# Kernel optimization log

Hardware: AMD Instinct MI355X
Metric: run time of the kernel (lower is better)

Reference implementation:

```python
import jax, jax.numpy as jnp
import numpy as np

N_CELL, N_WELL = 200000, 512
E_CC, E_CW = 1600000, 65536
CF, WF, ED, H = 12, 8, 1, 64
NEG_SLOPE = 0.2


def _p(k, shape, fan_in):
    return jax.random.normal(k, shape, jnp.float32) * (1.0 / np.sqrt(fan_in))


def setup_inputs() -> dict:
    key = jax.random.key(0)
    ks = jax.random.split(key, 32)
    d = {}
    d['cell_x'] = jax.random.normal(ks[0], (N_CELL, CF), jnp.float32)
    d['well_x'] = jax.random.normal(ks[1], (N_WELL, WF), jnp.float32)
    d['c2c_edge_attr'] = jax.random.normal(ks[2], (E_CC, ED), jnp.float32)
    d['c2c_edge_index'] = jax.random.randint(ks[3], (2, E_CC), 0, N_CELL)
    cw_src = jax.random.randint(ks[4], (E_CW,), 0, N_CELL)
    cw_dst = jax.random.randint(ks[5], (E_CW,), 0, N_WELL)
    d['c2w_edge_index'] = jnp.stack([cw_src, cw_dst])
    d['W_cell_emb'] = _p(ks[6], (CF, H), CF)
    d['b_cell_emb'] = jnp.zeros((H,), jnp.float32)
    d['W_well_emb'] = _p(ks[7], (WF, H), WF)
    d['b_well_emb'] = jnp.zeros((H,), jnp.float32)
    d['W_edge_emb'] = _p(ks[8], (ED, H), ED)
    d['b_edge_emb'] = jnp.zeros((H,), jnp.float32)
    d['conv_lin'] = _p(ks[9], (3, H, H), H)
    d['conv_lin_edge'] = _p(ks[10], (3, H, H), H)
    d['conv_att_src'] = _p(ks[11], (3, H), H)
    d['conv_att_dst'] = _p(ks[12], (3, H), H)
    d['conv_att_edge'] = _p(ks[13], (3, H), H)
    d['conv_bias'] = jnp.zeros((3, H), jnp.float32)
    d['wc_lin'] = _p(ks[14], (H, H), H)
    d['wc_att_src'] = _p(ks[15], (H,), H)
    d['wc_att_dst'] = _p(ks[16], (H,), H)
    d['wc_bias'] = jnp.zeros((H,), jnp.float32)
    d['mlp_W1'] = _p(ks[17], (H, H), H)
    d['mlp_b1'] = jnp.zeros((H,), jnp.float32)
    d['mlp_W2'] = _p(ks[18], (H, 75), H)
    d['mlp_b2'] = jnp.zeros((75,), jnp.float32)
    return d


def segment_softmax(logits, seg, num_segments):
    m = jax.ops.segment_max(logits, seg, num_segments=num_segments)
    m = jnp.where(jnp.isfinite(m), m, 0.0)  # empty segments -> 0
    e = jnp.exp(logits - m[seg])
    s = jax.ops.segment_sum(e, seg, num_segments=num_segments)
    return e / s[seg]


def gat_layer(h_src, h_dst, src, dst, lin, att_s, att_d, bias, num_dst,
              edge_feat=None, lin_edge=None, att_e=None):
    # PyG GATConv, heads=1, concat=False, add_self_loops=False
    hs = h_src @ lin                      # [Ns, H]
    hd = hs if h_dst is h_src else h_dst @ lin
    alpha = (hs @ att_s)[src] + (hd @ att_d)[dst]  # [E]
    if edge_feat is not None:
        alpha = alpha + (edge_feat @ lin_edge) @ att_e
    alpha = jax.nn.leaky_relu(alpha, NEG_SLOPE)
    p = segment_softmax(alpha, dst, num_dst)       # scatter-softmax per dst
    out = jax.ops.segment_sum(hs[src] * p[:, None], dst, num_segments=num_dst)
    return out + bias


def reference(cell_x, well_x, c2c_edge_attr,
              W_cell_emb, b_cell_emb, W_well_emb, b_well_emb,
              W_edge_emb, b_edge_emb,
              conv_lin, conv_lin_edge, conv_att_src, conv_att_dst,
              conv_att_edge, conv_bias,
              wc_lin, wc_att_src, wc_att_dst, wc_bias,
              mlp_W1, mlp_b1, mlp_W2, mlp_b2,
              c2c_edge_index, c2w_edge_index):
    h_c = cell_x @ W_cell_emb + b_cell_emb
    h_w = well_x @ W_well_emb + b_well_emb
    ea = c2c_edge_attr @ W_edge_emb + b_edge_emb
    src, dst = c2c_edge_index[0], c2c_edge_index[1]
    n_cell = h_c.shape[0]
    for l in range(3):
        h_c = jax.nn.relu(
            gat_layer(h_c, h_c, src, dst, conv_lin[l], conv_att_src[l],
                      conv_att_dst[l], conv_bias[l], n_cell,
                      edge_feat=ea, lin_edge=conv_lin_edge[l],
                      att_e=conv_att_edge[l]))
    ws, wd = c2w_edge_index[0], c2w_edge_index[1]
    h_well = gat_layer(h_c, h_w, ws, wd, wc_lin, wc_att_src, wc_att_dst,
                       wc_bias, h_w.shape[0])
    out = jax.nn.relu(h_well @ mlp_W1 + mlp_b1) @ mlp_W2 + mlp_b2
    return out.reshape(-1, 3, 25)
```

## Files before the change

### kernel.cpp

```cpp
#include <hip/hip_runtime.h>
#include <hip/hip_fp16.h>
#include <math.h>

#define CCAP 32
#define OVF_CAP 8192

__device__ __forceinline__ float wsum(float v){
  #pragma unroll
  for (int o=32;o;o>>=1) v += __shfl_xor(v,o);
  return v;
}

__global__ void k_edge_scalars(const float* __restrict__ lin_edge,
                               const float* __restrict__ att_e,
                               const float* __restrict__ Wrow,
                               const float* __restrict__ bemb,
                               float* __restrict__ escal){
  int l = threadIdx.x >> 6, j = threadIdx.x & 63;
  float v = 0.f;
  for (int k=0;k<64;++k) v = fmaf(lin_edge[l*4096 + j*64 + k], att_e[l*64+k], v);
  float sv = wsum(Wrow[j]*v);
  float ov = wsum(bemb[j]*v);
  if (j==0){ escal[l]=sv; escal[3+l]=ov; }
}

__global__ void k_prepA(const float* __restrict__ W_cell, const float* __restrict__ b_cell,
                        const float* __restrict__ lin0, float* __restrict__ weff){
  int t = threadIdx.x;
  for (int o=t; o<832; o+=256){
    float acc = 0.f;
    if (o < 768){
      int r = o >> 6, c2 = o & 63;
      for (int c=0;c<64;++c) acc = fmaf(W_cell[r*64+c], lin0[c*64+c2], acc);
    } else {
      int c2 = o - 768;
      for (int c=0;c<64;++c) acc = fmaf(b_cell[c], lin0[c*64+c2], acc);
    }
    weff[o] = acc;
  }
}

__global__ void k_prepB(const float* __restrict__ W_well, const float* __restrict__ b_well,
                        const float* __restrict__ wc_lin, const float* __restrict__ att_d,
                        float* __restrict__ wprep){
  __shared__ float tmp[64];
  int t = threadIdx.x;
  if (t < 64){
    float a = 0.f;
    for (int c=0;c<64;++c) a = fmaf(wc_lin[t*64+c], att_d[c], a);
    tmp[t] = a;
  }
  __syncthreads();
  if (t < 9){
    float a = 0.f;
    if (t < 8){ for (int k=0;k<64;++k) a = fmaf(W_well[t*64+k], tmp[k], a); }
    else      { for (int k=0;k<64;++k) a = fmaf(b_well[k],     tmp[k], a); }
    wprep[t] = a;
  }
}

__global__ void k_well_ad2(const float* __restrict__ well_x, const float* __restrict__ wprep,
                           float* __restrict__ ad_w, int n){
  int w = blockIdx.x*blockDim.x + threadIdx.x;
  if (w >= n) return;
  float a = wprep[8];
  #pragma unroll
  for (int r=0;r<8;++r) a = fmaf(well_x[w*8+r], wprep[r], a);
  ad_w[w] = a;
}

__global__ void k_build_cc(const int* __restrict__ src, const int* __restrict__ dst,
                           const float* __restrict__ attr, int* __restrict__ deg,
                           int2* __restrict__ slot, int4* __restrict__ ovf,
                           int* __restrict__ n_ovf, int e){
  int stride = gridDim.x*blockDim.x;
  for (int i = blockIdx.x*blockDim.x + threadIdx.x; i < e; i += stride){
    int d = dst[i];
    int off = atomicAdd(&deg[d], 1);
    if (off < CCAP){
      slot[(d<<5) + off] = make_int2(src[i], __float_as_int(attr[i]));
    } else {
      int x = atomicAdd(n_ovf, 1);
      if (x < OVF_CAP) ovf[x] = make_int4(d, src[i], __float_as_int(attr[i]), 0);
    }
  }
}

__global__ void k_count_w(const int* __restrict__ dst, int* __restrict__ deg,
                          int* __restrict__ off, int e){
  int i = blockIdx.x*blockDim.x + threadIdx.x;
  if (i<e) off[i] = atomicAdd(&deg[dst[i]], 1);
}

__global__ void k_scan_single(const int* __restrict__ deg, int* __restrict__ rowptr, int n){
  __shared__ int sm[1024];
  int t = threadIdx.x;
  sm[t] = (t<n) ? deg[t] : 0; __syncthreads();
  for (int o=1;o<blockDim.x;o<<=1){
    int v = (t>=o)?sm[t-o]:0; __syncthreads();
    sm[t]+=v; __syncthreads();
  }
  if (t<n) rowptr[t+1]=sm[t];
  if (t==0) rowptr[0]=0;
}

__global__ void k_fill_w(const int* __restrict__ src, const int* __restrict__ dst,
                         const int* __restrict__ rowptr, const int* __restrict__ off,
                         int* __restrict__ slot, int e){
  int i = blockIdx.x*blockDim.x + threadIdx.x;
  if (i>=e) return;
  int d = dst[i];
  slot[rowptr[d] + off[i]] = src[i];
}

__global__ __launch_bounds__(256) void k_gemm64(
    const float* __restrict__ h, const float* __restrict__ W,
    const float* __restrict__ att_s, const float* __restrict__ att_d,
    __half* __restrict__ hs, float* __restrict__ as_, float* __restrict__ ad_, int n){
  __shared__ float Ws[64*64];
  __shared__ float hT[64][68];
  int t = threadIdx.x;
  int n0 = blockIdx.x * 64;
  #pragma unroll
  for (int i=t;i<4096;i+=256) Ws[i] = W[i];
  for (int i=t;i<1024;i+=256){
    int node = i >> 4, k4 = (i & 15) << 2;
    int gn = n0 + node;
    float4 v = (gn < n) ? *(const float4*)&h[(size_t)gn*64 + k4] : make_float4(0,0,0,0);
    hT[k4+0][node]=v.x; hT[k4+1][node]=v.y; hT[k4+2][node]=v.z; hT[k4+3][node]=v.w;
  }
  __syncthreads();
  int tx = t & 15, ty = t >> 4;
  int f4 = tx*4;
  float acc[4][4] = {};
  for (int k=0;k<64;++k){
    float4 wv = *(const float4*)&Ws[k*64 + f4];
    float4 hv = *(const float4*)&hT[k][ty*4];
    float hvv[4] = {hv.x,hv.y,hv.z,hv.w};
    float wvv[4] = {wv.x,wv.y,wv.z,wv.w};
    #pragma unroll
    for (int i=0;i<4;++i)
      #pragma unroll
      for (int j=0;j<4;++j)
        acc[i][j] = fmaf(hvv[i], wvv[j], acc[i][j]);
  }
  float4 s4 = *(const float4*)&att_s[f4];
  float4 d4 = *(const float4*)&att_d[f4];
  #pragma unroll
  for (int i=0;i<4;++i){
    int gn = n0 + ty*4 + i;
    if (gn < n){
      union { __half2 h2; unsigned u; } lo, hi;
      lo.h2 = __floats2half2_rn(acc[i][0], acc[i][1]);
      hi.h2 = __floats2half2_rn(acc[i][2], acc[i][3]);
      *(int2*)&hs[(size_t)gn*64 + f4] = make_int2((int)lo.u, (int)hi.u);
      float sv = acc[i][0]*s4.x + acc[i][1]*s4.y + acc[i][2]*s4.z + acc[i][3]*s4.w;
      float dv = acc[i][0]*d4.x + acc[i][1]*d4.y + acc[i][2]*d4.z + acc[i][3]*d4.w;
      #pragma unroll
      for (int o=8;o;o>>=1){ sv += __shfl_xor(sv,o); dv += __shfl_xor(dv,o); }
      if (tx==0){ as_[gn]=sv; ad_[gn]=dv; }
    }
  }
}

__global__ __launch_bounds__(256) void k_gemm_l0(
    const float* __restrict__ x, const float* __restrict__ weff,
    const float* __restrict__ att_s, const float* __restrict__ att_d,
    __half* __restrict__ hs, float* __restrict__ as_, float* __restrict__ ad_, int n){
  __shared__ float Ws[12*64];
  __shared__ float xT[12][68];
  int t = threadIdx.x;
  int n0 = blockIdx.x * 64;
  for (int i=t;i<768;i+=256){
    Ws[i] = weff[i];
    int node = i / 12, r = i - node*12;
    int gn = n0 + node;
    xT[r][node] = (gn < n) ? x[(size_t)gn*12 + r] : 0.f;
  }
  __syncthreads();
  int tx = t & 15, ty = t >> 4;
  int f4 = tx*4;
  float4 be = *(const float4*)&weff[768 + f4];
  float acc[4][4];
  #pragma unroll
  for (int i=0;i<4;++i){ acc[i][0]=be.x; acc[i][1]=be.y; acc[i][2]=be.z; acc[i][3]=be.w; }
  #pragma unroll
  for (int k=0;k<12;++k){
    float4 wv = *(const float4*)&Ws[k*64 + f4];
    float hvv[4];
    #pragma unroll
    for (int i=0;i<4;++i) hvv[i] = xT[k][ty*4+i];
    float wvv[4] = {wv.x,wv.y,wv.z,wv.w};
    #pragma unroll
    for (int i=0;i<4;++i)
      #pragma unroll
      for (int j=0;j<4;++j)
        acc[i][j] = fmaf(hvv[i], wvv[j], acc[i][j]);
  }
  float4 s4 = *(const float4*)&att_s[f4];
  float4 d4 = *(const float4*)&att_d[f4];
  #pragma unroll
  for (int i=0;i<4;++i){
    int gn = n0 + ty*4 + i;
    if (gn < n){
      union { __half2 h2; unsigned u; } lo, hi;
      lo.h2 = __floats2half2_rn(acc[i][0], acc[i][1]);
      hi.h2 = __floats2half2_rn(acc[i][2], acc[i][3]);
      *(int2*)&hs[(size_t)gn*64 + f4] = make_int2((int)lo.u, (int)hi.u);
      float sv = acc[i][0]*s4.x + acc[i][1]*s4.y + acc[i][2]*s4.z + acc[i][3]*s4.w;
      float dv = acc[i][0]*d4.x + acc[i][1]*d4.y + acc[i][2]*d4.z + acc[i][3]*d4.w;
      #pragma unroll
      for (int o=8;o;o>>=1){ sv += __shfl_xor(sv,o); dv += __shfl_xor(dv,o); }
      if (tx==0){ as_[gn]=sv; ad_[gn]=dv; }
    }
  }
}

template<bool RELU>
__global__ __launch_bounds__(256) void k_gat_agg3(
    const int* __restrict__ deg, const int2* __restrict__ slot,
    const int4* __restrict__ ovf, const int* __restrict__ n_ovf_p,
    const float* __restrict__ as_, const float* __restrict__ ad_,
    const __half* __restrict__ hs, const float* __restrict__ bias,
    const float* __restrict__ escal, int l,
    float* __restrict__ out, int n){
  int t = threadIdx.x;
  int g = t & 15;
  int node = blockIdx.x*16 + (t >> 4);
  if (node >= n) return;
  int degn = deg[node];
  float4 b4 = *(const float4*)&bias[g*4];
  if (degn == 0){
    float4 r = b4;
    if (RELU){ r.x=fmaxf(r.x,0.f); r.y=fmaxf(r.y,0.f); r.z=fmaxf(r.z,0.f); r.w=fmaxf(r.w,0.f); }
    *(float4*)&out[(size_t)node*64 + g*4] = r;
    return;
  }
  float se = escal[l], oe = escal[3+l];
  float adn = ad_[node];
  int cin = min(degn, CCAP);
  int sb = node << 5;
  float areg[2]; int sreg[2];
  float m = -1e30f;
  #pragma unroll
  for (int it=0; it<2; ++it){
    int k = it*16 + g;
    areg[it] = -1e30f; sreg[it] = 0;
    if (k < cin){
      int2 sv = slot[sb + k];
      float a = as_[sv.x] + adn;
      a = fmaf(__int_as_float(sv.y), se, a) + oe;
      a = (a >= 0.f) ? a : 0.2f*a;
      areg[it] = a; sreg[it] = sv.x;
      m = fmaxf(m, a);
    }
  }
  int no = 0;
  if (degn > CCAP) no = min(*n_ovf_p, OVF_CAP);
  for (int j=0;j<no;++j){
    int4 e = ovf[j];
    if (e.x == node){
      float a = as_[e.y] + adn;
      a = fmaf(__int_as_float(e.z), se, a) + oe;
      a = (a >= 0.f) ? a : 0.2f*a;
      m = fmaxf(m, a);
    }
  }
  #pragma unroll
  for (int o=8;o;o>>=1) m = fmaxf(m, __shfl_xor(m, o, 16));

  float sum = 0.f;
  float4 acc = make_float4(0.f,0.f,0.f,0.f);
  #pragma unroll
  for (int it=0; it<2; ++it){
    int base = it*16;
    if (base < cin){
      float p = (base + g < cin) ? __expf(areg[it] - m) : 0.f;
      sum += p;
      int cnt = min(16, cin - base);
      for (int j=0;j<cnt;j+=4){
        float pj[4]; int sj[4];
        int s0 = __shfl(sreg[it], j, 16);
        #pragma unroll
        for (int u=0;u<4;++u){
          int jj = j+u;
          bool act = (jj < cnt);
          pj[u] = act ? __shfl(p, jj, 16) : 0.f;
          int sv = __shfl(sreg[it], act ? jj : j, 16);
          sj[u] = act ? sv : s0;
        }
        int2 hb[4];
        #pragma unroll
        for (int u=0;u<4;++u) hb[u] = *(const int2*)&hs[(size_t)sj[u]*64 + g*4];
        #pragma unroll
        for (int u=0;u<4;++u){
          union { unsigned u32; __half2 h2; } a0, a1;
          a0.u32 = (unsigned)hb[u].x; a1.u32 = (unsigned)hb[u].y;
          float2 f0 = __half22float2(a0.h2);
          float2 f1 = __half22float2(a1.h2);
          acc.x = fmaf(f0.x, pj[u], acc.x);
          acc.y = fmaf(f0.y, pj[u], acc.y);
          acc.z = fmaf(f1.x, pj[u], acc.z);
          acc.w = fmaf(f1.y, pj[u], acc.w);
        }
      }
    }
  }
  for (int j=0;j<no;++j){
    int4 e = ovf[j];
    if (e.x == node){
      float a = as_[e.y] + adn;
      a = fmaf(__int_as_float(e.z), se, a) + oe;
      a = (a >= 0.f) ? a : 0.2f*a;
      float p = __expf(a - m);
      if (g == 0) sum += p;
      int2 hb = *(const int2*)&hs[(size_t)e.y*64 + g*4];
      union { unsigned u; __half2 h2; } a0, a1; a0.u = (unsigned)hb.x; a1.u = (unsigned)hb.y;
      float2 f0 = __half22float2(a0.h2);
      float2 f1 = __half22float2(a1.h2);
      acc.x = fmaf(f0.x, p, acc.x);
      acc.y = fmaf(f0.y, p, acc.y);
      acc.z = fmaf(f1.x, p, acc.z);
      acc.w = fmaf(f1.y, p, acc.w);
    }
  }
  #pragma unroll
  for (int o=8;o;o>>=1) sum += __shfl_xor(sum, o, 16);
  float4 r;
  r.x = acc.x/sum + b4.x;
  r.y = acc.y/sum + b4.y;
  r.z = acc.z/sum + b4.z;
  r.w = acc.w/sum + b4.w;
  if (RELU){ r.x=fmaxf(r.x,0.f); r.y=fmaxf(r.y,0.f); r.z=fmaxf(r.z,0.f); r.w=fmaxf(r.w,0.f); }
  *(float4*)&out[(size_t)node*64 + g*4] = r;
}

template<int NA>
__global__ __launch_bounds__(256) void k_gat_aggw(
    const int* __restrict__ rowptr, const int* __restrict__ slot1,
    float* __restrict__ alpha_ws,
    const float* __restrict__ as_, const float* __restrict__ ad_,
    const __half* __restrict__ hs, const float* __restrict__ bias,
    float* __restrict__ out, int n){
  int t = threadIdx.x;
  int g = t & 15;
  int node = blockIdx.x*16 + (t >> 4);
  if (node >= n) return;
  int beg = rowptr[node], end = rowptr[node+1];
  float4 b4 = *(const float4*)&bias[g*4];
  if (end == beg){
    *(float4*)&out[(size_t)node*64 + g*4] = b4;
    return;
  }
  float adn = ad_[node];
  float areg[NA]; int sreg[NA];
  float m = -1e30f;
  #pragma unroll
  for (int it=0; it<NA; ++it){
    int k = beg + it*16 + g;
    areg[it] = -1e30f; sreg[it] = 0;
    if (k < end){
      int s = slot1[k];
      float a = as_[s] + adn;
      a = (a >= 0.f) ? a : 0.2f*a;
      areg[it] = a; sreg[it] = s;
      m = fmaxf(m, a);
    }
  }
  for (int k = beg + NA*16 + g; k < end; k += 16){
    int s = slot1[k];
    float a = as_[s] + adn;
    a = (a >= 0.f) ? a : 0.2f*a;
    alpha_ws[k] = a;
    m = fmaxf(m, a);
  }
  #pragma unroll
  for (int o=8;o;o>>=1) m = fmaxf(m, __shfl_xor(m, o, 16));

  float sum = 0.f;
  float4 acc = make_float4(0.f,0.f,0.f,0.f);
  #pragma unroll
  for (int it=0; it<NA; ++it){
    int base = beg + it*16;
    if (base < end){
      float p = (base + g < end) ? __expf(areg[it] - m) : 0.f;
      sum += p;
      int cnt = min(16, end - base);
      for (int j=0;j<cnt;++j){
        float pj = __shfl(p, j, 16);
        int   sj = __shfl(sreg[it], j, 16);
        int2 hb = *(const int2*)&hs[(size_t)sj*64 + g*4];
        union { unsigned u; __half2 h2; } a0, a1; a0.u = (unsigned)hb.x; a1.u = (unsigned)hb.y;
        float2 f0 = __half22float2(a0.h2);
        float2 f1 = __half22float2(a1.h2);
        acc.x = fmaf(f0.x, pj, acc.x);
        acc.y = fmaf(f0.y, pj, acc.y);
        acc.z = fmaf(f1.x, pj, acc.z);
        acc.w = fmaf(f1.y, pj, acc.w);
      }
    }
  }
  for (int base = beg + NA*16; base < end; base += 16){
    int k = base + g;
    float p = 0.f; int s = 0;
    if (k < end){ s = slot1[k]; p = __expf(alpha_ws[k] - m); }
    sum += p;
    int cnt = min(16, end - base);
    for (int j=0;j<cnt;++j){
      float pj = __shfl(p, j, 16);
      int   sj = __shfl(s, j, 16);
      int2 hb = *(const int2*)&hs[(size_t)sj*64 + g*4];
      union { unsigned u; __half2 h2; } a0, a1; a0.u = (unsigned)hb.x; a1.u = (unsigned)hb.y;
      float2 f0 = __half22float2(a0.h2);
      float2 f1 = __half22float2(a1.h2);
      acc.x = fmaf(f0.x, pj, acc.x);
      acc.y = fmaf(f0.y, pj, acc.y);
      acc.z = fmaf(f1.x, pj, acc.z);
      acc.w = fmaf(f1.y, pj, acc.w);
    }
  }
  #pragma unroll
  for (int o=8;o;o>>=1) sum += __shfl_xor(sum, o, 16);
  float4 r;
  r.x = acc.x/sum + b4.x;
  r.y = acc.y/sum + b4.y;
  r.z = acc.z/sum + b4.z;
  r.w = acc.w/sum + b4.w;
  *(float4*)&out[(size_t)node*64 + g*4] = r;
}

__global__ __launch_bounds__(128) void k_mlp(const float* __restrict__ h_well,
    const float* __restrict__ W1, const float* __restrict__ b1,
    const float* __restrict__ W2, const float* __restrict__ b2,
    float* __restrict__ out, int n){
  __shared__ float hr[64]; __shared__ float h1[64];
  int w = blockIdx.x, t = threadIdx.x;
  if (t<64) hr[t] = h_well[w*64+t];
  __syncthreads();
  if (t<64){
    float a = b1[t];
    for (int k=0;k<64;++k) a = fmaf(hr[k], W1[k*64+t], a);
    h1[t] = fmaxf(a, 0.f);
  }
  __syncthreads();
  if (t<75){
    float a = b2[t];
    for (int k=0;k<64;++k) a = fmaf(h1[k], W2[k*75+t], a);
    out[w*75+t] = a;
  }
}

extern "C" void kernel_launch(void* const* d_in, const int* in_sizes, int n_in,
                              void* d_out, int out_size, void* d_ws, size_t ws_size,
                              hipStream_t stream){
  const float* cell_x = (const float*)d_in[0];
  const float* well_x = (const float*)d_in[1];
  const float* eattr  = (const float*)d_in[2];
  const int*   cc_idx = (const int*)d_in[3];
  const int*   cw_idx = (const int*)d_in[4];
  const float* W_cell = (const float*)d_in[5];
  const float* b_cell = (const float*)d_in[6];
  const float* W_well = (const float*)d_in[7];
  const float* b_well = (const float*)d_in[8];
  const float* W_edge = (const float*)d_in[9];
  const float* b_edge = (const float*)d_in[10];
  const float* conv_lin = (const float*)d_in[11];
  const float* conv_lin_edge = (const float*)d_in[12];
  const float* att_src = (const float*)d_in[13];
  const float* att_dst = (const float*)d_in[14];
  const float* att_edge = (const float*)d_in[15];
  const float* conv_bias = (const float*)d_in[16];
  const float* wc_lin = (const float*)d_in[17];
  const float* wc_att_src = (const float*)d_in[18];
  const float* wc_att_dst = (const float*)d_in[19];
  const float* wc_bias = (const float*)d_in[20];
  const float* mlp_W1 = (const float*)d_in[21];
  const float* mlp_b1 = (const float*)d_in[22];
  const float* mlp_W2 = (const float*)d_in[23];
  const float* mlp_b2 = (const float*)d_in[24];

  int n_cell = in_sizes[0]/12;
  int n_well = in_sizes[1]/8;
  int e_cc = in_sizes[2];
  int e_cw = in_sizes[4]/2;

  const int* cc_src = cc_idx;
  const int* cc_dst = cc_idx + e_cc;
  const int* cw_src = cw_idx;
  const int* cw_dst = cw_idx + e_cw;

  char* p = (char*)d_ws;
  auto alloc = [&](size_t bytes)->void*{
    void* r = (void*)p;
    p += (bytes + 255) & ~(size_t)255;
    return r;
  };
  float* h_cur = (float*)alloc((size_t)n_cell*64*4);
  __half* hs   = (__half*)alloc((size_t)n_cell*64*2);
  float* as_   = (float*)alloc((size_t)n_cell*4);
  float* ad_   = (float*)alloc((size_t)n_cell*4);
  int* deg     = (int*)alloc((size_t)n_cell*4);
  int2* slot2  = (int2*)alloc((size_t)n_cell*CCAP*8);
  int4* ovf    = (int4*)alloc((size_t)OVF_CAP*16);
  int* n_ovf   = (int*)alloc(256);
  float* ad_w  = (float*)alloc((size_t)n_well*4);
  int* wdeg    = (int*)alloc((size_t)n_well*4);
  int* wrowptr = (int*)alloc((size_t)(n_well+1)*4);
  int* woff    = (int*)alloc((size_t)e_cw*4);
  int* wslot   = (int*)alloc((size_t)e_cw*4);
  float* walpha= (float*)alloc((size_t)e_cw*4);
  float* h_well= (float*)alloc((size_t)n_well*64*4);
  float* escal = (float*)alloc(64);
  float* weff  = (float*)alloc(832*4);
  float* wprep = (float*)alloc(16*4);

  hipMemsetAsync(deg, 0, (size_t)n_cell*4, stream);
  hipMemsetAsync(wdeg, 0, (size_t)n_well*4, stream);
  hipMemsetAsync(n_ovf, 0, 4, stream);

  k_edge_scalars<<<1, 192, 0, stream>>>(conv_lin_edge, att_edge, W_edge, b_edge, escal);
  k_prepA<<<1, 256, 0, stream>>>(W_cell, b_cell, conv_lin, weff);
  k_prepB<<<1, 128, 0, stream>>>(W_well, b_well, wc_lin, wc_att_dst, wprep);

  int gB = (e_cc + 255)/256; if (gB > 2048) gB = 2048;
  k_build_cc<<<gB, 256, 0, stream>>>(cc_src, cc_dst, eattr, deg, slot2, ovf, n_ovf, e_cc);

  k_count_w<<<(e_cw+255)/256, 256, 0, stream>>>(cw_dst, wdeg, woff, e_cw);
  k_scan_single<<<1, 512, 0, stream>>>(wdeg, wrowptr, n_well);
  k_fill_w<<<(e_cw+255)/256, 256, 0, stream>>>(cw_src, cw_dst, wrowptr, woff, wslot, e_cw);

  k_gemm_l0<<<(n_cell+63)/64, 256, 0, stream>>>(cell_x, weff,
      att_src, att_dst, hs, as_, ad_, n_cell);
  k_gat_agg3<true><<<(n_cell+15)/16, 256, 0, stream>>>(deg, slot2, ovf, n_ovf,
      as_, ad_, hs, conv_bias, escal, 0, h_cur, n_cell);

  for (int l=1;l<3;++l){
    k_gemm64<<<(n_cell+63)/64, 256, 0, stream>>>(h_cur, conv_lin + l*4096,
        att_src + l*64, att_dst + l*64, hs, as_, ad_, n_cell);
    k_gat_agg3<true><<<(n_cell+15)/16, 256, 0, stream>>>(deg, slot2, ovf, n_ovf,
        as_, ad_, hs, conv_bias + l*64, escal, l, h_cur, n_cell);
  }

  k_gemm64<<<(n_cell+63)/64, 256, 0, stream>>>(h_cur, wc_lin, wc_att_src, wc_att_dst,
      hs, as_, ad_, n_cell);
  k_well_ad2<<<(n_well+255)/256, 256, 0, stream>>>(well_x, wprep, ad_w, n_well);
  k_gat_aggw<16><<<(n_well+15)/16, 256, 0, stream>>>(wrowptr, wslot,
      walpha, as_, ad_w, hs, wc_bias, h_well, n_well);

  k_mlp<<<n_well, 128, 0, stream>>>(h_well, mlp_W1, mlp_b1, mlp_W2, mlp_b2, (float*)d_out, n_well);
}
```

Baseline: 598.7 us.

## Use fp16 MFMA for 64x64 node GEMMs and store hidden state in half

Replaces the scalar FP32 64x64 GEMM with an MFMA 16x16x32 f16 kernel that stages the node tile and the transposed weights in LDS as fp16. The aggregation kernel now writes the hidden state h_cur as fp16 instead of fp32. This halves the bytes written by aggregation and read by the GEMM, and moves the GEMM arithmetic onto matrix cores. In exchange, hidden activations and weights lose precision because they are quantized to fp16. The epilogue also switches from vectorized int2 stores to scalar half stores.

```diff
diff --git a/kernel.cpp b/kernel.cpp
--- a/kernel.cpp
+++ b/kernel.cpp
@@ -4,6 +4,9 @@
 
 #define CCAP 32
 #define OVF_CAP 8192
+
+typedef __attribute__((ext_vector_type(8))) _Float16 f16x8;
+typedef __attribute__((ext_vector_type(4))) float f32x4;
 
 __device__ __forceinline__ float wsum(float v){
   #pragma unroll
@@ -113,30 +116,96 @@
   slot[rowptr[d] + off[i]] = src[i];
 }
 
-__global__ __launch_bounds__(256) void k_gemm64(
-    const float* __restrict__ h, const float* __restrict__ W,
+__global__ __launch_bounds__(256) void k_gemm64m(
+    const __half* __restrict__ h, const float* __restrict__ W,
     const float* __restrict__ att_s, const float* __restrict__ att_d,
     __half* __restrict__ hs, float* __restrict__ as_, float* __restrict__ ad_, int n){
-  __shared__ float Ws[64*64];
-  __shared__ float hT[64][68];
+  __shared__ _Float16 hT[64][72];
+  __shared__ _Float16 wT[64][72];
   int t = threadIdx.x;
   int n0 = blockIdx.x * 64;
-  #pragma unroll
-  for (int i=t;i<4096;i+=256) Ws[i] = W[i];
-  for (int i=t;i<1024;i+=256){
-    int node = i >> 4, k4 = (i & 15) << 2;
+  for (int i=t; i<1024; i+=256){
+    int k = i >> 4, f4 = (i & 15) << 2;
+    float4 w4 = *(const float4*)&W[k*64 + f4];
+    wT[f4+0][k] = (_Float16)w4.x;
+    wT[f4+1][k] = (_Float16)w4.y;
+    wT[f4+2][k] = (_Float16)w4.z;
+    wT[f4+3][k] = (_Float16)w4.w;
+  }
+  for (int i=t; i<512; i+=256){
+    int node = i >> 3, c8 = (i & 7) << 3;
     int gn = n0 + node;
-    float4 v = (gn < n) ? *(const float4*)&h[(size_t)gn*64 + k4] : make_float4(0,0,0,0);
-    hT[k4+0][node]=v.x; hT[k4+1][node]=v.y; hT[k4+2][node]=v.z; hT[k4+3][node]=v.w;
+    if (gn < n){
+      *(f16x8*)&hT[node][c8] = *(const f16x8*)&h[(size_t)gn*64 + c8];
+    } else {
+      f16x8 z = {0,0,0,0,0,0,0,0};
+      *(f16x8*)&hT[node][c8] = z;
+    }
+  }
+  __syncthreads();
+  int w = t >> 6, lane = t & 63;
+  int lr = lane & 15, lg = lane >> 4;
+  f32x4 acc[4];
+  #pragma unroll
+  for (int c=0;c<4;++c) acc[c] = (f32x4){0.f,0.f,0.f,0.f};
+  #pragma unroll
+  for (int kk=0; kk<2; ++kk){
+    f16x8 a = *(const f16x8*)&hT[16*w + lr][kk*32 + lg*8];
+    #pragma unroll
+    for (int c=0;c<4;++c){
+      f16x8 b = *(const f16x8*)&wT[16*c + lr][kk*32 + lg*8];
+      acc[c] = __builtin_amdgcn_mfma_f32_16x16x32_f16(a, b, acc[c], 0, 0, 0);
+    }
+  }
+  float s_att[4], d_att[4];
+  #pragma unroll
+  for (int c=0;c<4;++c){ s_att[c]=att_s[16*c+lr]; d_att[c]=att_d[16*c+lr]; }
+  #pragma unroll
+  for (int r=0;r<4;++r){
+    int gn = n0 + 16*w + lg*4 + r;
+    float sv=0.f, dv=0.f;
+    if (gn < n){
+      #pragma unroll
+      for (int c=0;c<4;++c){
+        float v = acc[c][r];
+        hs[(size_t)gn*64 + 16*c + lr] = __float2half(v);
+        sv = fmaf(v, s_att[c], sv);
+        dv = fmaf(v, d_att[c], dv);
+      }
+    }
+    #pragma unroll
+    for (int o=8;o;o>>=1){ sv += __shfl_xor(sv,o,16); dv += __shfl_xor(dv,o,16); }
+    if (gn < n && lr==0){ as_[gn]=sv; ad_[gn]=dv; }
+  }
+}
+
+__global__ __launch_bounds__(256) void k_gemm_l0(
+    const float* __restrict__ x, const float* __restrict__ weff,
+    const float* __restrict__ att_s, const float* __restrict__ att_d,
+    __half* __restrict__ hs, float* __restrict__ as_, float* __restrict__ ad_, int n){
+  __shared__ float Ws[12*64];
+  __shared__ float xT[12][68];
+  int t = threadIdx.x;
+  int n0 = blockIdx.x * 64;
+  for (int i=t;i<768;i+=256){
+    Ws[i] = weff[i];
+    int node = i / 12, r = i - node*12;
+    int gn = n0 + node;
+    xT[r][node] = (gn < n) ? x[(size_t)gn*12 + r] : 0.f;
   }
   __syncthreads();
   int tx = t & 15, ty = t >> 4;
   int f4 = tx*4;
-  float acc[4][4] = {};
-  for (int k=0;k<64;++k){
+  float4 be = *(const float4*)&weff[768 + f4];
+  float acc[4][4];
+  #pragma unroll
+  for (int i=0;i<4;++i){ acc[i][0]=be.x; acc[i][1]=be.y; acc[i][2]=be.z; acc[i][3]=be.w; }
+  #pragma unroll
+  for (int k=0;k<12;++k){
     float4 wv = *(const float4*)&Ws[k*64 + f4];
-    float4 hv = *(const float4*)&hT[k][ty*4];
-    float hvv[4] = {hv.x,hv.y,hv.z,hv.w};
+    float hvv[4];
+    #pragma unroll
+    for (int i=0;i<4;++i) hvv[i] = xT[k][ty*4+i];
     float wvv[4] = {wv.x,wv.y,wv.z,wv.w};
     #pragma unroll
     for (int i=0;i<4;++i)
@@ -163,59 +232,6 @@
   }
 }
 
-__global__ __launch_bounds__(256) void k_gemm_l0(
-    const float* __restrict__ x, const float* __restrict__ weff,
-    const float* __restrict__ att_s, const float* __restrict__ att_d,
-    __half* __restrict__ hs, float* __restrict__ as_, float* __restrict__ ad_, int n){
-  __shared__ float Ws[12*64];
-  __shared__ float xT[12][68];
-  int t = threadIdx.x;
-  int n0 = blockIdx.x * 64;
-  for (int i=t;i<768;i+=256){
-    Ws[i] = weff[i];
-    int node = i / 12, r = i - node*12;
-    int gn = n0 + node;
-    xT[r][node] = (gn < n) ? x[(size_t)gn*12 + r] : 0.f;
-  }
-  __syncthreads();
-  int tx = t & 15, ty = t >> 4;
-  int f4 = tx*4;
-  float4 be = *(const float4*)&weff[768 + f4];
-  float acc[4][4];
-  #pragma unroll
-  for (int i=0;i<4;++i){ acc[i][0]=be.x; acc[i][1]=be.y; acc[i][2]=be.z; acc[i][3]=be.w; }
-  #pragma unroll
-  for (int k=0;k<12;++k){
-    float4 wv = *(const float4*)&Ws[k*64 + f4];
-    float hvv[4];
-    #pragma unroll
-    for (int i=0;i<4;++i) hvv[i] = xT[k][ty*4+i];
-    float wvv[4] = {wv.x,wv.y,wv.z,wv.w};
-    #pragma unroll
-    for (int i=0;i<4;++i)
-      #pragma unroll
-      for (int j=0;j<4;++j)
-        acc[i][j] = fmaf(hvv[i], wvv[j], acc[i][j]);
-  }
-  float4 s4 = *(const float4*)&att_s[f4];
-  float4 d4 = *(const float4*)&att_d[f4];
-  #pragma unroll
-  for (int i=0;i<4;++i){
-    int gn = n0 + ty*4 + i;
-    if (gn < n){
-      union { __half2 h2; unsigned u; } lo, hi;
-      lo.h2 = __floats2half2_rn(acc[i][0], acc[i][1]);
-      hi.h2 = __floats2half2_rn(acc[i][2], acc[i][3]);
-      *(int2*)&hs[(size_t)gn*64 + f4] = make_int2((int)lo.u, (int)hi.u);
-      float sv = acc[i][0]*s4.x + acc[i][1]*s4.y + acc[i][2]*s4.z + acc[i][3]*s4.w;
-      float dv = acc[i][0]*d4.x + acc[i][1]*d4.y + acc[i][2]*d4.z + acc[i][3]*d4.w;
-      #pragma unroll
-      for (int o=8;o;o>>=1){ sv += __shfl_xor(sv,o); dv += __shfl_xor(dv,o); }
-      if (tx==0){ as_[gn]=sv; ad_[gn]=dv; }
-    }
-  }
-}
-
 template<bool RELU>
 __global__ __launch_bounds__(256) void k_gat_agg3(
     const int* __restrict__ deg, const int2* __restrict__ slot,
@@ -223,7 +239,7 @@
     const float* __restrict__ as_, const float* __restrict__ ad_,
     const __half* __restrict__ hs, const float* __restrict__ bias,
     const float* __restrict__ escal, int l,
-    float* __restrict__ out, int n){
+    __half* __restrict__ out, int n){
   int t = threadIdx.x;
   int g = t & 15;
   int node = blockIdx.x*16 + (t >> 4);
@@ -233,7 +249,10 @@
   if (degn == 0){
     float4 r = b4;
     if (RELU){ r.x=fmaxf(r.x,0.f); r.y=fmaxf(r.y,0.f); r.z=fmaxf(r.z,0.f); r.w=fmaxf(r.w,0.f); }
-    *(float4*)&out[(size_t)node*64 + g*4] = r;
+    union { __half2 h2[2]; int2 i2; } u;
+    u.h2[0] = __floats2half2_rn(r.x, r.y);
+    u.h2[1] = __floats2half2_rn(r.z, r.w);
+    *(int2*)&out[(size_t)node*64 + g*4] = u.i2;
     return;
   }
   float se = escal[l], oe = escal[3+l];
@@ -332,7 +351,10 @@
   r.z = acc.z/sum + b4.z;
   r.w = acc.w/sum + b4.w;
   if (RELU){ r.x=fmaxf(r.x,0.f); r.y=fmaxf(r.y,0.f); r.z=fmaxf(r.z,0.f); r.w=fmaxf(r.w,0.f); }
-  *(float4*)&out[(size_t)node*64 + g*4] = r;
+  union { __half2 h2[2]; int2 i2; } u;
+  u.h2[0] = __floats2half2_rn(r.x, r.y);
+  u.h2[1] = __floats2half2_rn(r.z, r.w);
+  *(int2*)&out[(size_t)node*64 + g*4] = u.i2;
 }
 
 template<int NA>
@@ -495,7 +517,7 @@
     p += (bytes + 255) & ~(size_t)255;
     return r;
   };
-  float* h_cur = (float*)alloc((size_t)n_cell*64*4);
+  __half* h_cur = (__half*)alloc((size_t)n_cell*64*2);
   __half* hs   = (__half*)alloc((size_t)n_cell*64*2);
   float* as_   = (float*)alloc((size_t)n_cell*4);
   float* ad_   = (float*)alloc((size_t)n_cell*4);
@@ -535,13 +557,13 @@
       as_, ad_, hs, conv_bias, escal, 0, h_cur, n_cell);
 
   for (int l=1;l<3;++l){
-    k_gemm64<<<(n_cell+63)/64, 256, 0, stream>>>(h_cur, conv_lin + l*4096,
+    k_gemm64m<<<(n_cell+63)/64, 256, 0, stream>>>(h_cur, conv_lin + l*4096,
         att_src + l*64, att_dst + l*64, hs, as_, ad_, n_cell);
     k_gat_agg3<true><<<(n_cell+15)/16, 256, 0, stream>>>(deg, slot2, ovf, n_ovf,
         as_, ad_, hs, conv_bias + l*64, escal, l, h_cur, n_cell);
   }
 
-  k_gemm64<<<(n_cell+63)/64, 256, 0, stream>>>(h_cur, wc_lin, wc_att_src, wc_att_dst,
+  k_gemm64m<<<(n_cell+63)/64, 256, 0, stream>>>(h_cur, wc_lin, wc_att_src, wc_att_dst,
       hs, as_, ad_, n_cell);
   k_well_ad2<<<(n_well+255)/256, 256, 0, stream>>>(well_x, wprep, ad_w, n_well);
   k_gat_aggw<16><<<(n_well+15)/16, 256, 0, stream>>>(wrowptr, wslot,
```

Result: faster. 534.1 us (-10.8%).
